# Optimization experiments

Hardware: AMD Instinct MI355X
Metric: run time of the kernel (lower is better)

The kernel has to match this reference:

```python
import jax, jax.numpy as jnp
import numpy as np
from jax import lax

MAX_T = 1.0
MAX_Z = float(np.e)  # exp(MAX_T)
BITS = 8


def weight_quantization(w):
    # tanh -> scale by max-abs (no grad through alpha) -> clamp -> round with STE
    w = jnp.tanh(w)
    alpha = lax.stop_gradient(jnp.max(jnp.abs(w)))
    q = 2 ** (BITS - 1) - 1
    w = jnp.clip(w / alpha, -1.0, 1.0) * q
    w = w + lax.stop_gradient(jnp.round(w) - w)
    return w * alpha / q


def t_linear_c(inp, W, max_spike_time):
    # inp: [B, L, Fin], W: [Fout, Fin] -> out: [B, L, Fout]
    idx = jnp.argsort(inp, axis=-1)                              # [B,L,Fin]
    s_inp = jnp.take_along_axis(inp, idx, axis=-1)[..., None]    # [B,L,Fin,1]
    w_sorted = W.T[idx]                                          # [B,L,Fin,Fout]
    w_sorted = weight_quantization(w_sorted)
    mul = s_inp * w_sorted
    w_sum = jnp.cumsum(w_sorted, axis=-2)
    iw_sum = jnp.cumsum(mul, axis=-2)
    out_all = iw_sum / jnp.clip(w_sum - 1.0, 1e-10, 1e10)
    o = jnp.where(w_sum < 1.0, max_spike_time, out_all)
    o = jnp.where(o < s_inp, max_spike_time, o)
    nxt = jnp.concatenate([s_inp[:, :, 1:, :], jnp.ones_like(s_inp[:, :, :1, :])], axis=2)
    o = jnp.where(o > nxt, max_spike_time, o)
    return jnp.min(o, axis=-2)


def t_linear(inp, W, max_spike_time):
    # inp: [B, Fin], W: [Fout, Fin] -> out: [B, Fout]
    idx = jnp.argsort(inp, axis=-1)
    s_inp = jnp.take_along_axis(inp, idx, axis=-1)[..., None]    # [B,Fin,1]
    w_sorted = W.T[idx]                                          # [B,Fin,Fout]
    mul = s_inp * w_sorted
    w_sum = jnp.cumsum(w_sorted, axis=1)
    iw_sum = jnp.cumsum(mul, axis=1)
    out_all = iw_sum / jnp.clip(w_sum - 1.0, 1e-10, 1e10)
    o = jnp.where(w_sum < 1.0, max_spike_time, out_all)
    o = jnp.where(o < s_inp, max_spike_time, o)
    nxt = jnp.concatenate([s_inp[:, 1:, :], jnp.ones_like(s_inp[:, :1, :])], axis=1)
    o = jnp.where(o >= nxt, max_spike_time, o)  # note: >= in t_Linear (vs > in t_Linear_c)
    return jnp.min(o, axis=1)


def unfold(x, k, p, s):
    # torch F.unfold: zero-pad, extract kxk patches; feature order (C, kh, kw)
    B, C, H, W = x.shape
    xp = jnp.pad(x, ((0, 0), (0, 0), (p, p), (p, p)))
    oh = (H + 2 * p - k) // s + 1
    ow = (W + 2 * p - k) // s + 1
    ri = (jnp.arange(oh) * s)[:, None] + jnp.arange(k)           # [oh,k]
    ci = (jnp.arange(ow) * s)[:, None] + jnp.arange(k)           # [ow,k]
    pt = xp[:, :, ri[:, None, :, None], ci[None, :, None, :]]    # [B,C,oh,ow,k,k]
    pt = pt.transpose(0, 2, 3, 1, 4, 5).reshape(B, oh * ow, C * k * k)
    return pt, oh, ow


def t_conv(x, W, k, pad, stride, max_spike_time):
    B = x.shape[0]
    patches, oh, ow = unfold(x, k, pad, stride)                  # [B,L,C*k*k]
    patches = jnp.where(patches < 0.1, max_spike_time, patches)
    out = t_linear_c(patches, W, max_spike_time)                 # [B,L,Cout]
    return out.transpose(0, 2, 1).reshape(B, W.shape[0], oh, ow)


def max_pool2(x):
    return lax.reduce_window(x, -jnp.inf, lax.max, (1, 1, 2, 2), (1, 1, 2, 2), 'VALID')


def min_pool3(x):
    # -MaxPool3x3(stride 2)(-ConstantPad2d(1, 1e5)(x))
    xp = jnp.pad(x, ((0, 0), (0, 0), (1, 1), (1, 1)), constant_values=1e5)
    return -lax.reduce_window(-xp, -jnp.inf, lax.max, (1, 1, 3, 3), (1, 1, 2, 2), 'VALID')


def setup_inputs() -> dict:
    key = jax.random.key(0)
    ks = jax.random.split(key, 8)
    B = 8
    inp = jax.random.normal(ks[0], (B, 1, 64, 64), dtype=jnp.float32)
    conv1_w = jax.random.normal(ks[1], (32, 1, 5, 5), dtype=jnp.float32) * (1.0 / 5.0)
    bn_g = jnp.ones((32,), jnp.float32)
    bn_b = jnp.zeros((32,), jnp.float32)
    bn_m = jnp.zeros((32,), jnp.float32)
    bn_v = jnp.ones((32,), jnp.float32)
    def uw(k, fout, fin):
        return jax.random.uniform(k, (fout, fin), jnp.float32, 0.0, 10.0 / fin)
    w2 = uw(ks[2], 32, 3 * 3 * 32)
    w3 = uw(ks[3], 32, 3 * 3 * 32)
    w4 = uw(ks[4], 64, 3 * 3 * 32)
    w5 = uw(ks[5], 64, 3 * 3 * 64)
    w_fc = uw(ks[6], 10, 8 * 8 * 64)
    return {"inp": inp, "conv1_w": conv1_w, "bn_g": bn_g, "bn_b": bn_b,
            "bn_m": bn_m, "bn_v": bn_v, "w2": w2, "w3": w3, "w4": w4,
            "w5": w5, "w_fc": w_fc}


def reference(inp, conv1_w, bn_g, bn_b, bn_m, bn_v, w2, w3, w4, w5, w_fc):
    x = lax.conv_general_dilated(inp, conv1_w, (1, 1), ((2, 2), (2, 2)),
                                 dimension_numbers=('NCHW', 'OIHW', 'NCHW'))
    x = (x - bn_m[None, :, None, None]) * (bn_g / jnp.sqrt(bn_v + 1e-5))[None, :, None, None] \
        + bn_b[None, :, None, None]
    x = jax.nn.relu(x)
    x = max_pool2(x)                       # [B,32,32,32]
    x = jnp.minimum(x, MAX_T)
    z1 = jnp.exp(x)
    z2 = t_conv(z1, w2, 3, 1, 2, MAX_Z)    # [B,32,16,16]
    z3 = t_conv(z2, w3, 3, 1, 1, MAX_Z)    # [B,32,16,16]
    z3c = z3 * min_pool3(z1)
    z4 = t_conv(z3c, w4, 3, 1, 2, MAX_Z * 2)  # [B,64,8,8]
    z5 = t_conv(z4, w5, 3, 1, 1, MAX_Z * 2)   # [B,64,8,8]
    pm = min_pool3(z3c)                       # [B,32,8,8]
    pm = jnp.concatenate([pm, pm], axis=1)    # [B,64,8,8]
    z5c = (z5 * pm).reshape(z5.shape[0], -1)  # [B,4096]
    return t_linear(z5c, w_fc, MAX_Z * 4)     # [B,10]
```

## Files before the change

kernel.cpp:

```cpp
#include <hip/hip_runtime.h>
#include <hip/hip_bf16.h>
#include <math.h>

#define E32 2.7182817459106445f

__device__ __forceinline__ unsigned long long packkey(float vf, int idx) {
  unsigned u = __float_as_uint(vf);
  u = (u & 0x80000000u) ? ~u : (u | 0x80000000u);
  return (((unsigned long long)u) << 32) | (unsigned)idx;
}
__device__ __forceinline__ float unpackval(unsigned long long k) {
  unsigned m = (unsigned)(k >> 32);
  m = (m & 0x80000000u) ? (m ^ 0x80000000u) : ~m;
  return __uint_as_float(m);
}

__global__ __launch_bounds__(256) void tanh_max_kernel(
    const float* __restrict__ w2, const float* __restrict__ w3,
    const float* __restrict__ w4, const float* __restrict__ w5,
    float* __restrict__ tanhbuf, float* __restrict__ partials) {
  int blk = blockIdx.x;
  const float* w; int base_blk, tbase;
  if (blk < 36)       { w = w2; base_blk = 0;   tbase = 0; }
  else if (blk < 72)  { w = w3; base_blk = 36;  tbase = 9216; }
  else if (blk < 144) { w = w4; base_blk = 72;  tbase = 18432; }
  else                { w = w5; base_blk = 144; tbase = 36864; }
  int i = (blk - base_blk) * 256 + threadIdx.x;
  float t = tanhf(w[i]);
  tanhbuf[tbase + i] = t;
  __shared__ float red[256];
  red[threadIdx.x] = fabsf(t);
  __syncthreads();
  for (int s = 128; s > 0; s >>= 1) {
    if (threadIdx.x < s) red[threadIdx.x] = fmaxf(red[threadIdx.x], red[threadIdx.x + s]);
    __syncthreads();
  }
  if (threadIdx.x == 0) partials[blk] = red[0];
}

__global__ __launch_bounds__(256) void quant2_kernel(
    const float* __restrict__ tanhbuf, const float* __restrict__ partials,
    float* __restrict__ q2, float* __restrict__ q3,
    float* __restrict__ q4, float* __restrict__ q5) {
  int blk = blockIdx.x;
  float* dst; int base_blk, tbase, pb0, pb1, F, N;
  if (blk < 36)       { dst = q2; base_blk = 0;   tbase = 0;     pb0 = 0;   pb1 = 36;  F = 32; N = 288; }
  else if (blk < 72)  { dst = q3; base_blk = 36;  tbase = 9216;  pb0 = 36;  pb1 = 72;  F = 32; N = 288; }
  else if (blk < 144) { dst = q4; base_blk = 72;  tbase = 18432; pb0 = 72;  pb1 = 144; F = 64; N = 288; }
  else                { dst = q5; base_blk = 144; tbase = 36864; pb0 = 144; pb1 = 288; F = 64; N = 576; }
  __shared__ float red[256];
  float mx = 0.0f;
  for (int j = pb0 + threadIdx.x; j < pb1; j += 256) mx = fmaxf(mx, partials[j]);
  red[threadIdx.x] = mx;
  __syncthreads();
  for (int s = 128; s > 0; s >>= 1) {
    if (threadIdx.x < s) red[threadIdx.x] = fmaxf(red[threadIdx.x], red[threadIdx.x + s]);
    __syncthreads();
  }
  float a = red[0];
  int i = (blk - base_blk) * 256 + threadIdx.x;
  float t = tanhbuf[tbase + i];
  int f = i / N, n = i % N;
  float r = fminf(fmaxf(t / a, -1.0f), 1.0f) * 127.0f;
  dst[n * F + f] = rintf(r) * a / 127.0f;
}

__global__ __launch_bounds__(256) void transpose_wfc_kernel(
    const float* __restrict__ wfc, float* __restrict__ wfcT) {
  int o = blockIdx.x * 256 + threadIdx.x;
  if (o >= 40960) return;
  int n = o / 10, f = o % 10;
  wfcT[o] = wfc[f * 4096 + n];
}

__global__ __launch_bounds__(256) void conv1_kernel(
    const float* __restrict__ inp, const float* __restrict__ w,
    const float* __restrict__ g, const float* __restrict__ bb,
    const float* __restrict__ m, const float* __restrict__ vv,
    float* __restrict__ z1) {
  int idx = blockIdx.x * 256 + threadIdx.x;
  if (idx >= 8 * 32 * 32 * 32) return;
  int x = idx & 31, y = (idx >> 5) & 31, c = (idx >> 10) & 31, b = idx >> 15;
  float scale = g[c] / sqrtf(vv[c] + 1e-5f);
  float bias = bb[c];
  float mean = m[c];
  float mx = -3.402823466e38f;
  for (int dy = 0; dy < 2; ++dy) {
    for (int dx = 0; dx < 2; ++dx) {
      int oy = 2 * y + dy, ox = 2 * x + dx;
      float acc = 0.0f;
      for (int kh = 0; kh < 5; ++kh) {
        int r = oy + kh - 2;
        if (r < 0 || r >= 64) continue;
        for (int kw = 0; kw < 5; ++kw) {
          int cc2 = ox + kw - 2;
          if (cc2 < 0 || cc2 >= 64) continue;
          acc += w[c * 25 + kh * 5 + kw] * inp[(b * 64 + r) * 64 + cc2];
        }
      }
      float xs = (acc - mean) * scale + bias;
      xs = fmaxf(xs, 0.0f);
      mx = fmaxf(mx, xs);
    }
  }
  mx = fminf(mx, 1.0f);
  z1[idx] = (mx == 1.0f) ? E32 : expf(mx);
}

__global__ __launch_bounds__(256) void mp3_kernel(
    const float* __restrict__ in, float* __restrict__ out, int BC, int H) {
  int OH = H >> 1;
  int total = BC * OH * OH;
  int idx = blockIdx.x * 256 + threadIdx.x;
  if (idx >= total) return;
  int j = idx % OH, i = (idx / OH) % OH, bc = idx / (OH * OH);
  float mn = 100000.0f;
  for (int di = 0; di < 3; ++di) {
    int r = 2 * i - 1 + di;
    if (r < 0 || r >= H) continue;
    for (int dj = 0; dj < 3; ++dj) {
      int cc = 2 * j - 1 + dj;
      if (cc < 0 || cc >= H) continue;
      mn = fminf(mn, in[bc * H * H + r * H + cc]);
    }
  }
  out[idx] = mn;
}

__global__ __launch_bounds__(256) void mp3mul_kernel(
    const float* __restrict__ a, const float* __restrict__ b2,
    float* __restrict__ out, int BC, int H) {
  int OH = H >> 1;
  int total = BC * OH * OH;
  int idx = blockIdx.x * 256 + threadIdx.x;
  if (idx >= total) return;
  int j = idx % OH, i = (idx / OH) % OH, bc = idx / (OH * OH);
  float mn = 100000.0f;
  for (int di = 0; di < 3; ++di) {
    int r = 2 * i - 1 + di;
    if (r < 0 || r >= H) continue;
    for (int dj = 0; dj < 3; ++dj) {
      int cc = 2 * j - 1 + dj;
      if (cc < 0 || cc >= H) continue;
      int q = bc * H * H + r * H + cc;
      mn = fminf(mn, __fmul_rn(a[q], b2[q]));
    }
  }
  out[idx] = mn;
}

template <int CIN, int F, int S, int HIN, bool MUL, int T>
__global__ __launch_bounds__(T, 1) void tconv_kernel(
    const float* __restrict__ in, const float* __restrict__ in2,
    const float* __restrict__ wqt, float* __restrict__ out, float MST) {
  constexpr int N = CIN * 9;
  constexpr int OH = (HIN - 1) / S + 1;
  constexpr int P = OH * OH;
  constexpr int K = (N + T - 1) / T;
  constexpr int NCH = N / 32;

  __shared__ unsigned long long pk[N];
  __shared__ float sval[N + 1];
  __shared__ unsigned short sidx[N];
  __shared__ float wbuf[2][32 * F];
  __shared__ float wc[NCH][F];
  __shared__ float iwc[NCH][F];
  __shared__ float pmin[F * NCH];

  int blk = blockIdx.x;
  int b = blk / P, p = blk % P;
  int ph = p / OH, pw = p % OH;
  int tid = threadIdx.x;

  for (int n = tid; n < N; n += T) {
    int c = n / 9, kk = n % 9, kh = kk / 3, kw = kk % 3;
    int r = ph * S + kh - 1, cc = pw * S + kw - 1;
    float v = 0.0f;
    if (r >= 0 && r < HIN && cc >= 0 && cc < HIN) {
      int q = ((b * CIN + c) * HIN + r) * HIN + cc;
      v = MUL ? __fmul_rn(in[q], in2[q]) : in[q];
    }
    pk[n] = packkey((v < 0.1f) ? MST : v, n);
  }
  if (tid == 0) sval[N] = 1.0f;
  __syncthreads();

  unsigned long long mine[K];
  int rnk[K];
#pragma unroll
  for (int k = 0; k < K; ++k) {
    int i = tid + T * k;
    mine[k] = (i < N) ? pk[i] : ~0ull;
    rnk[k] = 0;
  }
  for (int j0 = 0; j0 < N; j0 += 8) {
    unsigned long long u[8];
#pragma unroll
    for (int r = 0; r < 8; ++r) u[r] = pk[j0 + r];
#pragma unroll
    for (int r = 0; r < 8; ++r) {
#pragma unroll
      for (int k = 0; k < K; ++k) rnk[k] += (u[r] < mine[k]) ? 1 : 0;
    }
  }
#pragma unroll
  for (int k = 0; k < K; ++k) {
    int i = tid + T * k;
    if (i < N) {
      sval[rnk[k]] = unpackval(mine[k]);
      sidx[rnk[k]] = (unsigned short)(mine[k] & 0xffffull);
    }
  }
  __syncthreads();

  for (int t = tid; t < 32 * F; t += T) {
    int q = t / F, f = t % F;
    wbuf[0][t] = wqt[(int)sidx[q] * F + f];
  }
  __syncthreads();

  float wsum = 0.0f, iwsum = 0.0f;
  for (int c = 0; c < NCH; ++c) {
    if (tid >= 64 && c + 1 < NCH) {
      int i0n = (c + 1) * 32;
      float* nb = wbuf[(c + 1) & 1];
      for (int t = tid - 64; t < 32 * F; t += (T - 64)) {
        int q = t / F, f = t % F;
        nb[t] = wqt[(int)sidx[i0n + q] * F + f];
      }
    }
    if (tid < F) {
      const float* wb = wbuf[c & 1];
      wc[c][tid] = wsum;
      iwc[c][tid] = iwsum;
      int i0 = c * 32;
#pragma unroll
      for (int q0 = 0; q0 < 32; q0 += 8) {
        float w8[8], s8[8];
#pragma unroll
        for (int r = 0; r < 8; ++r) {
          w8[r] = wb[(q0 + r) * F + tid];
          s8[r] = sval[i0 + q0 + r];
        }
#pragma unroll
        for (int r = 0; r < 8; ++r) {
          wsum = __fadd_rn(wsum, w8[r]);
          iwsum = __fadd_rn(iwsum, __fmul_rn(s8[r], w8[r]));
        }
      }
    }
    __syncthreads();
  }

  for (int task = tid; task < NCH * F; task += T) {
    int c = task / F, f = task % F;
    float ws = wc[c][f], iws = iwc[c][f], omin = 3.402823466e38f;
    int i0 = c * 32;
#pragma unroll
    for (int q0 = 0; q0 < 32; q0 += 8) {
      float wv8[8], sv8[8], nv8[8];
#pragma unroll
      for (int r = 0; r < 8; ++r) {
        int i = i0 + q0 + r;
        wv8[r] = wqt[(int)sidx[i] * F + f];
        sv8[r] = sval[i];
        nv8[r] = sval[i + 1];
      }
#pragma unroll
      for (int r = 0; r < 8; ++r) {
        ws = __fadd_rn(ws, wv8[r]);
        iws = __fadd_rn(iws, __fmul_rn(sv8[r], wv8[r]));
        float den = fminf(fmaxf(__fadd_rn(ws, -1.0f), 1e-10f), 1e10f);
        float oa = iws / den;
        float o = (ws < 1.0f) ? MST : oa;
        o = (o < sv8[r]) ? MST : o;
        o = (o > nv8[r]) ? MST : o;
        omin = fminf(omin, o);
      }
    }
    pmin[f * NCH + c] = omin;
  }
  __syncthreads();

  if (tid < F) {
    float m2 = pmin[tid * NCH];
#pragma unroll
    for (int c = 1; c < NCH; ++c) m2 = fminf(m2, pmin[tid * NCH + c]);
    out[(b * F + tid) * P + p] = m2;
  }
}

template <int LK, int LJ>
__device__ __forceinline__ void bpass(unsigned long long (&k)[8],
                                      unsigned long long* keys,
                                      int tid, int lane) {
  if constexpr (LJ >= 9) {
    constexpr int pm = 1 << (LJ - 3);
#pragma unroll
    for (int m = 0; m < 8; ++m) keys[m * 512 + tid] = k[m];
    __syncthreads();
    bool lower = ((tid & pm) == 0);
    bool up = (((tid >> (LK - 3)) & 1) == 0);
    bool wmin = (lower == up);
#pragma unroll
    for (int m = 0; m < 8; ++m) {
      unsigned long long o = keys[m * 512 + (tid ^ pm)];
      unsigned long long mine = k[m];
      k[m] = wmin ? (mine < o ? mine : o) : (mine > o ? mine : o);
    }
    __syncthreads();
  } else if constexpr (LJ >= 3) {
    constexpr int lm = 1 << (LJ - 3);
    bool lower = ((lane & lm) == 0);
    bool up = (((tid >> (LK - 3)) & 1) == 0);
    bool wmin = (lower == up);
#pragma unroll
    for (int m = 0; m < 8; ++m) {
      unsigned long long o = __shfl_xor(k[m], lm, 64);
      unsigned long long mine = k[m];
      k[m] = wmin ? (mine < o ? mine : o) : (mine > o ? mine : o);
    }
  } else {
    constexpr int j = 1 << LJ;
#pragma unroll
    for (int m = 0; m < 8; ++m) {
      if ((m & j) == 0) {
        int i = (tid << 3) + m;
        bool up = (((i >> LK) & 1) == 0);
        unsigned long long a = k[m], c2 = k[m | j];
        if ((a > c2) == up) { k[m] = c2; k[m | j] = a; }
      }
    }
  }
}

template <int LK, int LJ>
__device__ __forceinline__ void bpasses(unsigned long long (&k)[8],
                                        unsigned long long* keys,
                                        int tid, int lane) {
  bpass<LK, LJ>(k, keys, tid, lane);
  if constexpr (LJ > 0) bpasses<LK, LJ - 1>(k, keys, tid, lane);
}

template <int LK>
__device__ __forceinline__ void bstages(unsigned long long (&k)[8],
                                        unsigned long long* keys,
                                        int tid, int lane) {
  bpasses<LK, LK - 1>(k, keys, tid, lane);
  if constexpr (LK < 12) bstages<LK + 1>(k, keys, tid, lane);
}

__global__ __launch_bounds__(512, 1) void fc_kernel(
    const float* __restrict__ z5, const float* __restrict__ m3,
    const float* __restrict__ wfcT, float* __restrict__ out) {
  constexpr int NN = 4096;
  __shared__ __align__(16) unsigned long long keys[NN];
  __shared__ __align__(16) float sval[NN + 1];
  __shared__ __align__(16) unsigned short sidx[NN];
  __shared__ float wc[64][10];
  __shared__ float iwc[64][10];
  __shared__ float pmin[64][10];
  float* wsA = (float*)keys;
  float* wsB = (float*)keys + 2608;

  int b = blockIdx.x, tid = threadIdx.x;
  int lane = tid & 63;

  {
    const float4* w4 = (const float4*)wfcT;
    float4 pf[20];
#pragma unroll
    for (int u = 0; u < 20; ++u) pf[u] = w4[tid + u * 512];
#pragma unroll
    for (int u = 0; u < 20; ++u)
      asm volatile("" :: "v"(pf[u].x), "v"(pf[u].y), "v"(pf[u].z), "v"(pf[u].w));
  }

  unsigned long long k[8];
  {
    int c = tid >> 3, p0 = (tid << 3) & 63;
    const float4* z4p = (const float4*)(z5 + (b * 64 + c) * 64 + p0);
    const float4* m4p = (const float4*)(m3 + (b * 32 + (c & 31)) * 64 + p0);
    float4 za = z4p[0], zb = z4p[1], ma = m4p[0], mb = m4p[1];
    int n0 = tid << 3;
    k[0] = packkey(__fmul_rn(za.x, ma.x), n0 + 0);
    k[1] = packkey(__fmul_rn(za.y, ma.y), n0 + 1);
    k[2] = packkey(__fmul_rn(za.z, ma.z), n0 + 2);
    k[3] = packkey(__fmul_rn(za.w, ma.w), n0 + 3);
    k[4] = packkey(__fmul_rn(zb.x, mb.x), n0 + 4);
    k[5] = packkey(__fmul_rn(zb.y, mb.y), n0 + 5);
    k[6] = packkey(__fmul_rn(zb.z, mb.z), n0 + 6);
    k[7] = packkey(__fmul_rn(zb.w, mb.w), n0 + 7);
  }

  bstages<1>(k, keys, tid, lane);

  {
    float4 v0, v1;
    v0.x = unpackval(k[0]); v0.y = unpackval(k[1]);
    v0.z = unpackval(k[2]); v0.w = unpackval(k[3]);
    v1.x = unpackval(k[4]); v1.y = unpackval(k[5]);
    v1.z = unpackval(k[6]); v1.w = unpackval(k[7]);
    ((float4*)sval)[tid * 2] = v0;
    ((float4*)sval)[tid * 2 + 1] = v1;
    ushort si[8];
#pragma unroll
    for (int m = 0; m < 8; ++m) si[m] = (unsigned short)(k[m] & 0xffffull);
    ((ulong2*)sidx)[tid] = *(ulong2*)si;
  }
  if (tid == 0) sval[NN] = 1.0f;
  __syncthreads();

  {
    float tmp[5];
#pragma unroll
    for (int u = 0; u < 5; ++u) {
      int t = tid + u * 512;
      tmp[u] = wfcT[(int)sidx[t / 10] * 10 + (t % 10)];
    }
#pragma unroll
    for (int u = 0; u < 5; ++u) {
      int t = tid + u * 512;
      wsA[(t % 10) * 260 + t / 10] = tmp[u];
    }
  }
  __syncthreads();

  float wsum = 0.0f, iwsum = 0.0f;
  for (int c = 0; c < 16; ++c) {
    int c0 = c * 256;
    float* cur = (c & 1) ? wsB : wsA;
    float* nxt = (c & 1) ? wsA : wsB;
    if (tid >= 64 && c + 1 < 16) {
      int c0n = c0 + 256;
      float tmp[6];
#pragma unroll
      for (int u = 0; u < 6; ++u) {
        int t = (tid - 64) + u * 448;
        tmp[u] = (t < 2560) ? wfcT[(int)sidx[c0n + t / 10] * 10 + (t % 10)] : 0.0f;
      }
#pragma unroll
      for (int u = 0; u < 6; ++u) {
        int t = (tid - 64) + u * 448;
        if (t < 2560) nxt[(t % 10) * 260 + t / 10] = tmp[u];
      }
    }
    if (tid < 10) {
      const float* wrow = cur + tid * 260;
      float4 wA4[4], sA4[4], wB4[4], sB4[4];
      auto LD = [&](int i0, float4* w4, float4* s4) {
#pragma unroll
        for (int kq = 0; kq < 4; ++kq) {
          w4[kq] = *(const float4*)(wrow + i0 + 4 * kq);
          s4[kq] = *(const float4*)(sval + c0 + i0 + 4 * kq);
        }
      };
      auto ACC = [&](const float4* w4, const float4* s4) {
#pragma unroll
        for (int kq = 0; kq < 4; ++kq) {
          float w0 = w4[kq].x, w1 = w4[kq].y, w2 = w4[kq].z, w3 = w4[kq].w;
          float s0 = s4[kq].x, s1 = s4[kq].y, s2 = s4[kq].z, s3 = s4[kq].w;
          wsum = __fadd_rn(wsum, w0); iwsum = __fadd_rn(iwsum, __fmul_rn(s0, w0));
          wsum = __fadd_rn(wsum, w1); iwsum = __fadd_rn(iwsum, __fmul_rn(s1, w1));
          wsum = __fadd_rn(wsum, w2); iwsum = __fadd_rn(iwsum, __fmul_rn(s2, w2));
          wsum = __fadd_rn(wsum, w3); iwsum = __fadd_rn(iwsum, __fmul_rn(s3, w3));
        }
      };
      LD(0, wA4, sA4);
      for (int i0 = 0; i0 < 256; i0 += 32) {
        if ((i0 & 63) == 0) {
          int cc = (c0 + i0) >> 6;
          wc[cc][tid] = wsum;
          iwc[cc][tid] = iwsum;
        }
        LD(i0 + 16, wB4, sB4);
        ACC(wA4, sA4);
        if (i0 + 32 < 256) LD(i0 + 32, wA4, sA4);
        ACC(wB4, sB4);
      }
    }
    __syncthreads();
  }

  const float MST = 4.0f * E32;
  for (int task = tid; task < 640; task += 512) {
    int c = task / 10, f = task % 10;
    float wsr = wc[c][f], iwsr = iwc[c][f], omin = 3.402823466e38f;
    int i0 = c * 64;
    for (int q0 = 0; q0 < 64; q0 += 8) {
      float wv8[8], sv8[8], nv8[8];
#pragma unroll
      for (int r = 0; r < 8; ++r) {
        int i = i0 + q0 + r;
        wv8[r] = wfcT[(int)sidx[i] * 10 + f];
        sv8[r] = sval[i];
        nv8[r] = sval[i + 1];
      }
#pragma unroll
      for (int r = 0; r < 8; ++r) {
        wsr = __fadd_rn(wsr, wv8[r]);
        iwsr = __fadd_rn(iwsr, __fmul_rn(sv8[r], wv8[r]));
        float den = fminf(fmaxf(__fadd_rn(wsr, -1.0f), 1e-10f), 1e10f);
        float oa = iwsr / den;
        float o = (wsr < 1.0f) ? MST : oa;
        o = (o < sv8[r]) ? MST : o;
        o = (o >= nv8[r]) ? MST : o;
        omin = fminf(omin, o);
      }
    }
    pmin[c][f] = omin;
  }
  __syncthreads();

  if (tid < 10) {
    float m = pmin[0][tid];
#pragma unroll
    for (int c = 1; c < 64; ++c) m = fminf(m, pmin[c][tid]);
    out[b * 10 + tid] = m;
  }
}

extern "C" void kernel_launch(void* const* d_in, const int* in_sizes, int n_in,
                              void* d_out, int out_size, void* d_ws, size_t ws_size,
                              hipStream_t stream) {
  const float* inp   = (const float*)d_in[0];
  const float* w1    = (const float*)d_in[1];
  const float* bn_g  = (const float*)d_in[2];
  const float* bn_b  = (const float*)d_in[3];
  const float* bn_m  = (const float*)d_in[4];
  const float* bn_v  = (const float*)d_in[5];
  const float* w2    = (const float*)d_in[6];
  const float* w3    = (const float*)d_in[7];
  const float* w4    = (const float*)d_in[8];
  const float* w5    = (const float*)d_in[9];
  const float* wfc   = (const float*)d_in[10];
  float* out = (float*)d_out;

  float* ws = (float*)d_ws;
  float* wq2 = ws + 16;
  float* wq3 = wq2 + 9216;
  float* wq4 = wq3 + 9216;
  float* wq5 = wq4 + 18432;
  float* z1  = wq5 + 36864;
  float* m1  = z1 + 262144;
  float* z2  = m1 + 65536;
  float* z3  = z2 + 65536;
  float* m3  = z3 + 65536;
  float* z4  = m3 + 16384;
  float* z5  = z4 + 32768;
  float* tanhbuf  = z5 + 32768;
  float* partials = tanhbuf + 73728;
  float* wfcT = partials + 512;

  tanh_max_kernel<<<288, 256, 0, stream>>>(w2, w3, w4, w5, tanhbuf, partials);
  quant2_kernel<<<288, 256, 0, stream>>>(tanhbuf, partials, wq2, wq3, wq4, wq5);
  transpose_wfc_kernel<<<160, 256, 0, stream>>>(wfc, wfcT);

  conv1_kernel<<<1024, 256, 0, stream>>>(inp, w1, bn_g, bn_b, bn_m, bn_v, z1);
  mp3_kernel<<<256, 256, 0, stream>>>(z1, m1, 8 * 32, 32);

  tconv_kernel<32, 32, 2, 32, false, 320><<<8 * 256, 320, 0, stream>>>(z1, nullptr, wq2, z2, E32);
  tconv_kernel<32, 32, 1, 16, false, 320><<<8 * 256, 320, 0, stream>>>(z2, nullptr, wq3, z3, E32);
  mp3mul_kernel<<<64, 256, 0, stream>>>(z3, m1, m3, 8 * 32, 16);
  tconv_kernel<32, 64, 2, 16, true, 512><<<8 * 64, 512, 0, stream>>>(z3, m1, wq4, z4, 2.0f * E32);
  tconv_kernel<64, 64, 1, 8, false, 512><<<8 * 64, 512, 0, stream>>>(z4, nullptr, wq5, z5, 2.0f * E32);

  fc_kernel<<<8, 512, 0, stream>>>(z5, m3, wfcT, out);
}
```

Before: 252.0 us.

## Split FC kernel into separate sort and scan kernels with runtime-loop bitonic sort

Splits the fused FC kernel into a bitonic-sort kernel that writes sorted values and indices to global memory, and a scan kernel that reloads them and runs the cumulative weight scan. The compile-time template recursion for the sort becomes runtime loops, and the wfcT register prefetch is dropped. The likely aim is to cut register pressure and code size and give each phase its own shared-memory layout. In exchange it adds a kernel launch and a global round trip of the sorted data, and the runtime loop bounds may cost some unrolling.

```diff
diff --git a/kernel.cpp b/kernel.cpp
--- a/kernel.cpp
+++ b/kernel.cpp
@@ -290,91 +290,16 @@
   }
 }
 
-template <int LK, int LJ>
-__device__ __forceinline__ void bpass(unsigned long long (&k)[8],
-                                      unsigned long long* keys,
-                                      int tid, int lane) {
-  if constexpr (LJ >= 9) {
-    constexpr int pm = 1 << (LJ - 3);
-#pragma unroll
-    for (int m = 0; m < 8; ++m) keys[m * 512 + tid] = k[m];
-    __syncthreads();
-    bool lower = ((tid & pm) == 0);
-    bool up = (((tid >> (LK - 3)) & 1) == 0);
-    bool wmin = (lower == up);
-#pragma unroll
-    for (int m = 0; m < 8; ++m) {
-      unsigned long long o = keys[m * 512 + (tid ^ pm)];
-      unsigned long long mine = k[m];
-      k[m] = wmin ? (mine < o ? mine : o) : (mine > o ? mine : o);
-    }
-    __syncthreads();
-  } else if constexpr (LJ >= 3) {
-    constexpr int lm = 1 << (LJ - 3);
-    bool lower = ((lane & lm) == 0);
-    bool up = (((tid >> (LK - 3)) & 1) == 0);
-    bool wmin = (lower == up);
-#pragma unroll
-    for (int m = 0; m < 8; ++m) {
-      unsigned long long o = __shfl_xor(k[m], lm, 64);
-      unsigned long long mine = k[m];
-      k[m] = wmin ? (mine < o ? mine : o) : (mine > o ? mine : o);
-    }
-  } else {
-    constexpr int j = 1 << LJ;
-#pragma unroll
-    for (int m = 0; m < 8; ++m) {
-      if ((m & j) == 0) {
-        int i = (tid << 3) + m;
-        bool up = (((i >> LK) & 1) == 0);
-        unsigned long long a = k[m], c2 = k[m | j];
-        if ((a > c2) == up) { k[m] = c2; k[m | j] = a; }
-      }
-    }
-  }
-}
-
-template <int LK, int LJ>
-__device__ __forceinline__ void bpasses(unsigned long long (&k)[8],
-                                        unsigned long long* keys,
-                                        int tid, int lane) {
-  bpass<LK, LJ>(k, keys, tid, lane);
-  if constexpr (LJ > 0) bpasses<LK, LJ - 1>(k, keys, tid, lane);
-}
-
-template <int LK>
-__device__ __forceinline__ void bstages(unsigned long long (&k)[8],
-                                        unsigned long long* keys,
-                                        int tid, int lane) {
-  bpasses<LK, LK - 1>(k, keys, tid, lane);
-  if constexpr (LK < 12) bstages<LK + 1>(k, keys, tid, lane);
-}
-
-__global__ __launch_bounds__(512, 1) void fc_kernel(
+#define CE(x, y) { int i_ = (tid << 3) + (x); \
+  bool up_ = (((i_ >> lk) & 1) == 0); \
+  unsigned long long a_ = k[(x)], c_ = k[(y)]; \
+  if ((a_ > c_) == up_) { k[(x)] = c_; k[(y)] = a_; } }
+
+__global__ __launch_bounds__(512, 1) void fc_sort_kernel(
     const float* __restrict__ z5, const float* __restrict__ m3,
-    const float* __restrict__ wfcT, float* __restrict__ out) {
-  constexpr int NN = 4096;
-  __shared__ __align__(16) unsigned long long keys[NN];
-  __shared__ __align__(16) float sval[NN + 1];
-  __shared__ __align__(16) unsigned short sidx[NN];
-  __shared__ float wc[64][10];
-  __shared__ float iwc[64][10];
-  __shared__ float pmin[64][10];
-  float* wsA = (float*)keys;
-  float* wsB = (float*)keys + 2608;
-
-  int b = blockIdx.x, tid = threadIdx.x;
-  int lane = tid & 63;
-
-  {
-    const float4* w4 = (const float4*)wfcT;
-    float4 pf[20];
-#pragma unroll
-    for (int u = 0; u < 20; ++u) pf[u] = w4[tid + u * 512];
-#pragma unroll
-    for (int u = 0; u < 20; ++u)
-      asm volatile("" :: "v"(pf[u].x), "v"(pf[u].y), "v"(pf[u].z), "v"(pf[u].w));
-  }
+    float* __restrict__ svalG, unsigned short* __restrict__ sidxG) {
+  __shared__ __align__(16) unsigned long long keys[4096];
+  int b = blockIdx.x, tid = threadIdx.x, lane = tid & 63;
 
   unsigned long long k[8];
   {
@@ -393,7 +318,43 @@
     k[7] = packkey(__fmul_rn(zb.w, mb.w), n0 + 7);
   }
 
-  bstages<1>(k, keys, tid, lane);
+  for (int lk = 1; lk <= 12; ++lk) {
+    for (int lj = lk - 1; lj >= 0; --lj) {
+      if (lj >= 9) {
+        int pm = 1 << (lj - 3);
+#pragma unroll
+        for (int m = 0; m < 8; ++m) keys[m * 512 + tid] = k[m];
+        __syncthreads();
+        bool lower = ((tid & pm) == 0);
+        bool up = (((tid >> (lk - 3)) & 1) == 0);
+        bool wmin = (lower == up);
+#pragma unroll
+        for (int m = 0; m < 8; ++m) {
+          unsigned long long o = keys[m * 512 + (tid ^ pm)];
+          unsigned long long mine = k[m];
+          k[m] = wmin ? (mine < o ? mine : o) : (mine > o ? mine : o);
+        }
+        __syncthreads();
+      } else if (lj >= 3) {
+        int lm = 1 << (lj - 3);
+        bool lower = ((lane & lm) == 0);
+        bool up = (((tid >> (lk - 3)) & 1) == 0);
+        bool wmin = (lower == up);
+#pragma unroll
+        for (int m = 0; m < 8; ++m) {
+          unsigned long long o = __shfl_xor(k[m], lm, 64);
+          unsigned long long mine = k[m];
+          k[m] = wmin ? (mine < o ? mine : o) : (mine > o ? mine : o);
+        }
+      } else if (lj == 2) {
+        CE(0, 4) CE(1, 5) CE(2, 6) CE(3, 7)
+      } else if (lj == 1) {
+        CE(0, 2) CE(1, 3) CE(4, 6) CE(5, 7)
+      } else {
+        CE(0, 1) CE(2, 3) CE(4, 5) CE(6, 7)
+      }
+    }
+  }
 
   {
     float4 v0, v1;
@@ -401,14 +362,36 @@
     v0.z = unpackval(k[2]); v0.w = unpackval(k[3]);
     v1.x = unpackval(k[4]); v1.y = unpackval(k[5]);
     v1.z = unpackval(k[6]); v1.w = unpackval(k[7]);
-    ((float4*)sval)[tid * 2] = v0;
-    ((float4*)sval)[tid * 2 + 1] = v1;
+    float* svalRow = svalG + b * 4104;
+    ((float4*)svalRow)[tid * 2] = v0;
+    ((float4*)svalRow)[tid * 2 + 1] = v1;
     ushort si[8];
 #pragma unroll
     for (int m = 0; m < 8; ++m) si[m] = (unsigned short)(k[m] & 0xffffull);
-    ((ulong2*)sidx)[tid] = *(ulong2*)si;
-  }
-  if (tid == 0) sval[NN] = 1.0f;
+    ((ulong2*)(sidxG + b * 4096))[tid] = *(ulong2*)si;
+    if (tid == 0) svalRow[4096] = 1.0f;
+  }
+}
+#undef CE
+
+__global__ __launch_bounds__(512, 1) void fc_scan_kernel(
+    const float* __restrict__ svalG, const unsigned short* __restrict__ sidxG,
+    const float* __restrict__ wfcT, float* __restrict__ out) {
+  constexpr int NN = 4096;
+  __shared__ __align__(16) float sval[NN + 1];
+  __shared__ __align__(16) unsigned short sidx[NN];
+  __shared__ __align__(16) float wstage[2][2608];
+  __shared__ float wc[64][10];
+  __shared__ float iwc[64][10];
+  __shared__ float pmin[64][10];
+
+  int b = blockIdx.x, tid = threadIdx.x;
+  const float* svalRow = svalG + b * 4104;
+
+  for (int t = tid; t < 1024; t += 512)
+    ((float4*)sval)[t] = ((const float4*)svalRow)[t];
+  ((ulong2*)sidx)[tid] = ((const ulong2*)(sidxG + b * 4096))[tid];
+  if (tid == 0) sval[NN] = svalRow[4096];
   __syncthreads();
 
   {
@@ -421,7 +404,7 @@
 #pragma unroll
     for (int u = 0; u < 5; ++u) {
       int t = tid + u * 512;
-      wsA[(t % 10) * 260 + t / 10] = tmp[u];
+      wstage[0][(t % 10) * 260 + t / 10] = tmp[u];
     }
   }
   __syncthreads();
@@ -429,8 +412,8 @@
   float wsum = 0.0f, iwsum = 0.0f;
   for (int c = 0; c < 16; ++c) {
     int c0 = c * 256;
-    float* cur = (c & 1) ? wsB : wsA;
-    float* nxt = (c & 1) ? wsA : wsB;
+    const float* cur = wstage[c & 1];
+    float* nxt = wstage[(c & 1) ^ 1];
     if (tid >= 64 && c + 1 < 16) {
       int c0n = c0 + 256;
       float tmp[6];
@@ -551,6 +534,8 @@
   float* tanhbuf  = z5 + 32768;
   float* partials = tanhbuf + 73728;
   float* wfcT = partials + 512;
+  float* svalG = wfcT + 40960;
+  unsigned short* sidxG = (unsigned short*)(svalG + 32832);
 
   tanh_max_kernel<<<288, 256, 0, stream>>>(w2, w3, w4, w5, tanhbuf, partials);
   quant2_kernel<<<288, 256, 0, stream>>>(tanhbuf, partials, wq2, wq3, wq4, wq5);
@@ -565,5 +550,6 @@
   tconv_kernel<32, 64, 2, 16, true, 512><<<8 * 64, 512, 0, stream>>>(z3, m1, wq4, z4, 2.0f * E32);
   tconv_kernel<64, 64, 1, 8, false, 512><<<8 * 64, 512, 0, stream>>>(z4, nullptr, wq5, z5, 2.0f * E32);
 
-  fc_kernel<<<8, 512, 0, stream>>>(z5, m3, wfcT, out);
-}
+  fc_sort_kernel<<<8, 512, 0, stream>>>(z5, m3, svalG, sidxG);
+  fc_scan_kernel<<<8, 512, 0, stream>>>(svalG, sidxG, wfcT, out);
+}
```

New measurement: 265.2 us. +5.2%, slower.
